# Kernel optimization log

Hardware: AMD Instinct MI355X
Metric: run time of the kernel (lower is better)

Reference implementation:

```python
import jax, jax.numpy as jnp
import numpy as np

B = 32; H = 56; W = 56; DIM = 192; WS = 7; SHIFT = 3; HEADS = 6
HEAD_DIM = DIM // HEADS; N = WS * WS; NW = (H // WS) * (W // WS)
HIDDEN = int(DIM * 4.0)
EPS = 1e-5


def _rel_pos_index():
    # standard Swin relative position index, shape (N, N), static
    coords = np.stack(np.meshgrid(np.arange(WS), np.arange(WS), indexing='ij'))  # (2, ws, ws)
    coords = coords.reshape(2, -1)                                               # (2, N)
    rel = (coords[:, :, None] - coords[:, None, :]).transpose(1, 2, 0)           # (N, N, 2)
    rel[:, :, 0] += WS - 1
    rel[:, :, 1] += WS - 1
    rel[:, :, 0] *= 2 * WS - 1
    return rel.sum(-1)  # (N, N)

REL_IDX = _rel_pos_index()


def _compute_attn_mask():
    # standard Swin SW-MSA mask, shape (NW, N, N), static
    img = np.zeros((H, W), dtype=np.float32)
    cnt = 0
    slices = (slice(0, -WS), slice(-WS, -SHIFT), slice(-SHIFT, None))
    for hs in slices:
        for ws_ in slices:
            img[hs, ws_] = cnt
            cnt += 1
    mw = img.reshape(H // WS, WS, W // WS, WS).transpose(0, 2, 1, 3).reshape(-1, N)  # (NW, N)
    diff = mw[:, None, :] - mw[:, :, None]
    return np.where(diff != 0, np.float32(-100.0), np.float32(0.0))


def _layernorm(x, g, b):
    mu = jnp.mean(x, axis=-1, keepdims=True)
    var = jnp.mean(jnp.square(x - mu), axis=-1, keepdims=True)
    return (x - mu) * jax.lax.rsqrt(var + EPS) * g + b


def setup_inputs() -> dict:
    key = jax.random.key(0)
    ks = jax.random.split(key, 8)
    s = 0.02
    inp = {
        'x': jax.random.normal(ks[0], (B, H * W, DIM), dtype=jnp.float32),
        'g1': jnp.ones((DIM,), jnp.float32), 'b1': jnp.zeros((DIM,), jnp.float32),
        'qkv_w': jax.random.normal(ks[1], (DIM, 3 * DIM), jnp.float32) * s,
        'qkv_b': jnp.zeros((3 * DIM,), jnp.float32),
        'proj_w': jax.random.normal(ks[2], (DIM, DIM), jnp.float32) * s,
        'proj_b': jnp.zeros((DIM,), jnp.float32),
        'rel_table': jax.random.normal(ks[3], ((2 * WS - 1) ** 2, HEADS), jnp.float32) * s,
        'g2': jnp.ones((DIM,), jnp.float32), 'b2': jnp.zeros((DIM,), jnp.float32),
        'fc1_w': jax.random.normal(ks[4], (DIM, HIDDEN), jnp.float32) * s,
        'fc1_b': jnp.zeros((HIDDEN,), jnp.float32),
        'fc2_w': jax.random.normal(ks[5], (HIDDEN, DIM), jnp.float32) * s,
        'fc2_b': jnp.zeros((DIM,), jnp.float32),
        'attn_mask': jnp.asarray(_compute_attn_mask()),
    }
    return inp


def reference(x, g1, b1, qkv_w, qkv_b, proj_w, proj_b, rel_table, g2, b2,
              fc1_w, fc1_b, fc2_w, fc2_b, attn_mask):
    shortcut = x
    h = _layernorm(x, g1, b1).reshape(B, H, W, DIM)
    h = jnp.roll(h, (-SHIFT, -SHIFT), axis=(1, 2))
    # window partition -> (B*NW, N, C)
    win = h.reshape(B, H // WS, WS, W // WS, WS, DIM).transpose(0, 1, 3, 2, 4, 5)
    win = win.reshape(-1, N, DIM)
    qkv = (win @ qkv_w + qkv_b).reshape(-1, N, 3, HEADS, HEAD_DIM).transpose(2, 0, 3, 1, 4)
    q, k, v = qkv[0], qkv[1], qkv[2]                         # (B*NW, heads, N, d)
    attn = jnp.einsum('whnd,whmd->whnm', q, k) * (HEAD_DIM ** -0.5)
    bias = rel_table[REL_IDX.reshape(-1)].reshape(N, N, HEADS).transpose(2, 0, 1)
    attn = attn + bias[None]
    attn = attn.reshape(B, NW, HEADS, N, N) + attn_mask[None, :, None]
    attn = jax.nn.softmax(attn, axis=-1).reshape(-1, HEADS, N, N)
    out = jnp.einsum('whnm,whmd->whnd', attn, v).transpose(0, 2, 1, 3).reshape(-1, N, DIM)
    out = out @ proj_w + proj_b
    # window reverse -> (B, H, W, C)
    out = out.reshape(B, H // WS, W // WS, WS, WS, DIM).transpose(0, 1, 3, 2, 4, 5)
    out = out.reshape(B, H, W, DIM)
    out = jnp.roll(out, (SHIFT, SHIFT), axis=(1, 2)).reshape(B, H * W, DIM)
    x = shortcut + out
    shortcut2 = x
    h = _layernorm(x, g2, b2)
    h = jax.nn.gelu(h @ fc1_w + fc1_b, approximate=False)
    h = h @ fc2_w + fc2_b
    return shortcut2 + h
```

## Files before the change

kernel.cpp:

```cpp
#include <hip/hip_runtime.h>
#include <math.h>

#define B_      32
#define HH      56
#define WW_     56
#define DIM     192
#define WS_     7
#define SHIFT_  3
#define HEADS   6
#define HDIM    32
#define NTOK    49
#define NWIN    64
#define HIDDEN  768
#define MTOT    (B_*HH*WW_)
#define CHUNK2  50176
#define EPS_    1e-5f
#define SCALE_  0.17677669529663687f

#define BK  32
#define LDK 40

#define ALD 200
#define PLD 36
#define VLD 68

typedef unsigned short u16;
typedef __attribute__((ext_vector_type(8))) __bf16 bf16x8;
typedef __attribute__((ext_vector_type(4))) float f32x4;

__device__ __forceinline__ float bf2f(u16 u) {
    union { unsigned int i; float f; } c; c.i = ((unsigned int)u) << 16; return c.f;
}
__device__ __forceinline__ u16 f2bf(float f) {
    union { float f; unsigned int i; } c; c.f = f;
    unsigned int x = c.i;
    return (u16)((x + 0x7FFFu + ((x >> 16) & 1u)) >> 16);
}

__device__ __forceinline__ float wave_sum(float v) {
    #pragma unroll
    for (int off = 32; off > 0; off >>= 1) v += __shfl_xor(v, off, 64);
    return v;
}

__global__ __launch_bounds__(256) void transpose_w_kernel(
        const float* __restrict__ W, u16* __restrict__ Wt, int K, int N) {
    __shared__ float t[32][33];
    int nt32 = N >> 5;
    int bx = blockIdx.x % nt32;
    int by = blockIdx.x / nt32;
    int tx = threadIdx.x & 31, ty = threadIdx.x >> 5;
    #pragma unroll
    for (int i = 0; i < 4; i++)
        t[ty + i * 8][tx] = W[(size_t)(by * 32 + ty + i * 8) * N + bx * 32 + tx];
    __syncthreads();
    #pragma unroll
    for (int i = 0; i < 4; i++)
        Wt[(size_t)(bx * 32 + ty + i * 8) * K + by * 32 + tx] = f2bf(t[tx][ty + i * 8]);
}

__global__ __launch_bounds__(256) void build_tbl_kernel(
        const float* __restrict__ rel_table, const float* __restrict__ mask,
        float* __restrict__ tbl) {
    int idx = blockIdx.x * 256 + threadIdx.x;
    int kj   = idx & 63;
    int qi   = (idx >> 6) & 63;
    int head = (idx >> 12) % 6;
    int wl   = idx / (6 << 12);
    float v;
    if (qi < NTOK && kj < NTOK) {
        int qr = qi / WS_, qc = qi % WS_;
        int kr = kj / WS_, kc = kj % WS_;
        int ri = (qr - kr + 6) * 13 + (qc - kc + 6);
        v = rel_table[ri * HEADS + head] + mask[((size_t)wl * NTOK + qi) * NTOK + kj];
    } else {
        v = -1e30f;
    }
    tbl[idx] = v;
}

__global__ __launch_bounds__(256) void ln1_window_kernel(
        const float* __restrict__ x, const float* __restrict__ g,
        const float* __restrict__ b, u16* __restrict__ out) {
    int row  = blockIdx.x * 4 + (threadIdx.x >> 6);
    int lane = threadIdx.x & 63;
    int win = row / NTOK;
    int n   = row - win * NTOK;
    int bb  = win >> 6;
    int wl  = win & 63;
    int hi  = (wl >> 3) * WS_ + n / WS_;
    int hj  = (wl & 7) * WS_ + n % WS_;
    int sh = hi + SHIFT_; if (sh >= HH) sh -= HH;
    int sw = hj + SHIFT_; if (sw >= WW_) sw -= WW_;
    const float* xr = x + ((size_t)(bb * HH * WW_ + sh * WW_ + sw)) * DIM;
    float v0 = xr[lane], v1 = xr[lane + 64], v2 = xr[lane + 128];
    float s  = wave_sum(v0 + v1 + v2);
    float sq = wave_sum(v0 * v0 + v1 * v1 + v2 * v2);
    float mu  = s * (1.0f / DIM);
    float var = sq * (1.0f / DIM) - mu * mu;
    float r = rsqrtf(var + EPS_);
    u16* orow = out + (size_t)row * DIM;
    orow[lane]       = f2bf((v0 - mu) * r * g[lane]       + b[lane]);
    orow[lane + 64]  = f2bf((v1 - mu) * r * g[lane + 64]  + b[lane + 64]);
    orow[lane + 128] = f2bf((v2 - mu) * r * g[lane + 128] + b[lane + 128]);
}

__global__ __launch_bounds__(256) void ln2_kernel(
        const float* __restrict__ x, const float* __restrict__ g,
        const float* __restrict__ b, u16* __restrict__ out) {
    int row  = blockIdx.x * 4 + (threadIdx.x >> 6);
    int lane = threadIdx.x & 63;
    const float* xr = x + (size_t)row * DIM;
    float v0 = xr[lane], v1 = xr[lane + 64], v2 = xr[lane + 128];
    float s  = wave_sum(v0 + v1 + v2);
    float sq = wave_sum(v0 * v0 + v1 * v1 + v2 * v2);
    float mu  = s * (1.0f / DIM);
    float var = sq * (1.0f / DIM) - mu * mu;
    float r = rsqrtf(var + EPS_);
    u16* orow = out + (size_t)row * DIM;
    orow[lane]       = f2bf((v0 - mu) * r * g[lane]       + b[lane]);
    orow[lane + 64]  = f2bf((v1 - mu) * r * g[lane + 64]  + b[lane + 64]);
    orow[lane + 128] = f2bf((v2 - mu) * r * g[lane + 128] + b[lane + 128]);
}

__global__ __launch_bounds__(384) void fused_attn_kernel(
        const u16* __restrict__ hwin, const u16* __restrict__ qkv_wT,
        const float* __restrict__ qkv_b, const u16* __restrict__ proj_wT,
        const float* __restrict__ proj_b, const float* __restrict__ tbl,
        const float* __restrict__ x, float* __restrict__ x1) {
    __shared__ u16 sm[26880];
    u16* R1 = sm;
    u16* Vt = sm + 13824;

    const int tid  = threadIdx.x;
    const int w    = tid >> 6;
    const int lane = tid & 63;
    const int lrow = lane & 15, lq = lane >> 4;
    const int win  = blockIdx.x;
    const int wl   = win & 63, bb = win >> 6;

    {
        const uint4* src = (const uint4*)(hwin + (size_t)win * NTOK * DIM);
        uint4 z; z.x = z.y = z.z = z.w = 0u;
        #pragma unroll
        for (int it = 0; it < 4; it++) {
            int i = tid + it * 384;
            int row = i / 24, c = i - row * 24;
            uint4 v = (row < NTOK) ? src[row * 24 + c] : z;
            *(uint4*)&R1[row * ALD + c * 8] = v;
        }
    }
    __syncthreads();

    f32x4 acc[3][4][2];
    #pragma unroll
    for (int o = 0; o < 3; o++)
        #pragma unroll
        for (int mt = 0; mt < 4; mt++)
            #pragma unroll
            for (int nt = 0; nt < 2; nt++) acc[o][mt][nt] = (f32x4){0.f, 0.f, 0.f, 0.f};

    const u16* bcol[3][2];
    #pragma unroll
    for (int o = 0; o < 3; o++)
        #pragma unroll
        for (int nt = 0; nt < 2; nt++)
            bcol[o][nt] = qkv_wT + (size_t)(o * DIM + w * 32 + nt * 16 + lrow) * DIM + lq * 8;

    #pragma unroll
    for (int ks = 0; ks < 6; ks++) {
        bf16x8 aF[4];
        #pragma unroll
        for (int mt = 0; mt < 4; mt++)
            aF[mt] = *(const bf16x8*)&R1[(mt * 16 + lrow) * ALD + ks * 32 + lq * 8];
        bf16x8 bF[3][2];
        #pragma unroll
        for (int o = 0; o < 3; o++)
            #pragma unroll
            for (int nt = 0; nt < 2; nt++)
                bF[o][nt] = *(const bf16x8*)(bcol[o][nt] + ks * 32);
        __builtin_amdgcn_s_setprio(1);
        #pragma unroll
        for (int o = 0; o < 3; o++)
            #pragma unroll
            for (int mt = 0; mt < 4; mt++)
                #pragma unroll
                for (int nt = 0; nt < 2; nt++)
                    acc[o][mt][nt] = __builtin_amdgcn_mfma_f32_16x16x32_bf16(
                        aF[mt], bF[o][nt], acc[o][mt][nt], 0, 0, 0);
        __builtin_amdgcn_s_setprio(0);
    }
    float bias_[3][2];
    #pragma unroll
    for (int o = 0; o < 3; o++)
        #pragma unroll
        for (int nt = 0; nt < 2; nt++)
            bias_[o][nt] = qkv_b[o * DIM + w * 32 + nt * 16 + lrow];
    #pragma unroll
    for (int o = 0; o < 3; o++)
        #pragma unroll
        for (int mt = 0; mt < 4; mt++)
            #pragma unroll
            for (int nt = 0; nt < 2; nt++)
                #pragma unroll
                for (int r = 0; r < 4; r++) acc[o][mt][nt][r] += bias_[o][nt];

    __syncthreads();

    #pragma unroll
    for (int mt = 0; mt < 4; mt++)
        #pragma unroll
        for (int nt = 0; nt < 2; nt++)
            #pragma unroll
            for (int r = 0; r < 4; r++)
                R1[(mt * 16 + lq * 4 + r) * ALD + w * 32 + nt * 16 + lrow] =
                    f2bf(acc[0][mt][nt][r]);
    bf16x8 qf[4];
    #pragma unroll
    for (int mt = 0; mt < 4; mt++)
        qf[mt] = *(const bf16x8*)&R1[(mt * 16 + lrow) * ALD + w * 32 + lq * 8];

    #pragma unroll
    for (int mt = 0; mt < 4; mt++)
        #pragma unroll
        for (int nt = 0; nt < 2; nt++)
            #pragma unroll
            for (int r = 0; r < 4; r++)
                R1[(mt * 16 + lq * 4 + r) * ALD + w * 32 + nt * 16 + lrow] =
                    f2bf(acc[1][mt][nt][r]);
    bf16x8 kf[4];
    #pragma unroll
    for (int nt = 0; nt < 4; nt++)
        kf[nt] = *(const bf16x8*)&R1[(nt * 16 + lrow) * ALD + w * 32 + lq * 8];

    #pragma unroll
    for (int mt = 0; mt < 4; mt++)
        #pragma unroll
        for (int nt = 0; nt < 2; nt++)
            #pragma unroll
            for (int r = 0; r < 4; r++)
                Vt[(w * 32 + nt * 16 + lrow) * VLD + mt * 16 + lq * 4 + r] =
                    f2bf(acc[2][mt][nt][r]);

    f32x4 sc[4][4];
    __builtin_amdgcn_s_setprio(1);
    #pragma unroll
    for (int mt = 0; mt < 4; mt++)
        #pragma unroll
        for (int nt = 0; nt < 4; nt++) {
            f32x4 z = (f32x4){0.f, 0.f, 0.f, 0.f};
            sc[mt][nt] = __builtin_amdgcn_mfma_f32_16x16x32_bf16(qf[mt], kf[nt], z, 0, 0, 0);
        }
    __builtin_amdgcn_s_setprio(0);
    const float* tb = tbl + (((size_t)wl * HEADS + w) << 12);
    float inv[4][4];
    #pragma unroll
    for (int mt = 0; mt < 4; mt++)
        #pragma unroll
        for (int r = 0; r < 4; r++) {
            int qi = mt * 16 + lq * 4 + r;
            float mx = -3.0e38f;
            #pragma unroll
            for (int nt = 0; nt < 4; nt++) {
                float s = sc[mt][nt][r] * SCALE_ + tb[(qi << 6) + nt * 16 + lrow];
                sc[mt][nt][r] = s;
                mx = fmaxf(mx, s);
            }
            #pragma unroll
            for (int off = 8; off > 0; off >>= 1) mx = fmaxf(mx, __shfl_xor(mx, off, 64));
            float sum = 0.f;
            #pragma unroll
            for (int nt = 0; nt < 4; nt++) {
                float e = __expf(sc[mt][nt][r] - mx);
                sc[mt][nt][r] = e;
                sum += e;
            }
            #pragma unroll
            for (int off = 8; off > 0; off >>= 1) sum += __shfl_xor(sum, off, 64);
            inv[mt][r] = 1.0f / sum;
        }

    u16* Pl = R1 + w * (64 * PLD);
    f32x4 oc[4][2];
    #pragma unroll
    for (int mt = 0; mt < 4; mt++)
        #pragma unroll
        for (int nd = 0; nd < 2; nd++) oc[mt][nd] = (f32x4){0.f, 0.f, 0.f, 0.f};
    #pragma unroll
    for (int ks = 0; ks < 2; ks++) {
        #pragma unroll
        for (int mt = 0; mt < 4; mt++)
            #pragma unroll
            for (int ntl = 0; ntl < 2; ntl++)
                #pragma unroll
                for (int r = 0; r < 4; r++)
                    Pl[(mt * 16 + lq * 4 + r) * PLD + ntl * 16 + lrow] =
                        f2bf(sc[mt][ks * 2 + ntl][r]);
        bf16x8 vf[2];
        #pragma unroll
        for (int nd = 0; nd < 2; nd++)
            vf[nd] = *(const bf16x8*)&Vt[(w * 32 + nd * 16 + lrow) * VLD + ks * 32 + lq * 8];
        __builtin_amdgcn_s_setprio(1);
        #pragma unroll
        for (int mt = 0; mt < 4; mt++) {
            bf16x8 pf = *(const bf16x8*)&Pl[(mt * 16 + lrow) * PLD + lq * 8];
            #pragma unroll
            for (int nd = 0; nd < 2; nd++)
                oc[mt][nd] = __builtin_amdgcn_mfma_f32_16x16x32_bf16(pf, vf[nd],
                                                                     oc[mt][nd], 0, 0, 0);
        }
        __builtin_amdgcn_s_setprio(0);
    }
    __syncthreads();

    #pragma unroll
    for (int mt = 0; mt < 4; mt++)
        #pragma unroll
        for (int nd = 0; nd < 2; nd++)
            #pragma unroll
            for (int r = 0; r < 4; r++)
                R1[(mt * 16 + lq * 4 + r) * ALD + w * 32 + nd * 16 + lrow] =
                    f2bf(oc[mt][nd][r] * inv[mt][r]);
    __syncthreads();

    f32x4 pacc[4][2];
    #pragma unroll
    for (int mt = 0; mt < 4; mt++)
        #pragma unroll
        for (int nt = 0; nt < 2; nt++) pacc[mt][nt] = (f32x4){0.f, 0.f, 0.f, 0.f};
    const u16* pcol[2];
    #pragma unroll
    for (int nt = 0; nt < 2; nt++)
        pcol[nt] = proj_wT + (size_t)(w * 32 + nt * 16 + lrow) * DIM + lq * 8;
    #pragma unroll
    for (int ks = 0; ks < 6; ks++) {
        bf16x8 af[4];
        #pragma unroll
        for (int mt = 0; mt < 4; mt++)
            af[mt] = *(const bf16x8*)&R1[(mt * 16 + lrow) * ALD + ks * 32 + lq * 8];
        bf16x8 pb[2];
        #pragma unroll
        for (int nt = 0; nt < 2; nt++) pb[nt] = *(const bf16x8*)(pcol[nt] + ks * 32);
        __builtin_amdgcn_s_setprio(1);
        #pragma unroll
        for (int mt = 0; mt < 4; mt++)
            #pragma unroll
            for (int nt = 0; nt < 2; nt++)
                pacc[mt][nt] = __builtin_amdgcn_mfma_f32_16x16x32_bf16(
                    af[mt], pb[nt], pacc[mt][nt], 0, 0, 0);
        __builtin_amdgcn_s_setprio(0);
    }
    float pbias[2];
    #pragma unroll
    for (int nt = 0; nt < 2; nt++) pbias[nt] = proj_b[w * 32 + nt * 16 + lrow];
    #pragma unroll
    for (int mt = 0; mt < 4; mt++)
        #pragma unroll
        for (int r = 0; r < 4; r++) {
            int n = mt * 16 + lq * 4 + r;
            if (n < NTOK) {
                int hi = (wl >> 3) * WS_ + n / WS_;
                int hj = (wl & 7) * WS_ + n % WS_;
                int dh = hi + SHIFT_; if (dh >= HH) dh -= HH;
                int dw = hj + SHIFT_; if (dw >= WW_) dw -= WW_;
                size_t tok = (size_t)(bb * HH * WW_ + dh * WW_ + dw);
                #pragma unroll
                for (int nt = 0; nt < 2; nt++) {
                    int col = w * 32 + nt * 16 + lrow;
                    x1[tok * DIM + col] = x[tok * DIM + col] + pacc[mt][nt][r] + pbias[nt];
                }
            }
        }
}

template<int K, int BM_, int BN_, int WR, int MT>
__device__ __forceinline__ void gemm_core2(
        const u16* __restrict__ A, const u16* __restrict__ Bt,
        int m0, int n0, u16 (*As)[BM_][LDK], u16 (*Bs)[BN_][LDK],
        f32x4 (&acc)[MT][4]) {
    constexpr int WC = 4 / WR;
    constexpr int AL = BM_ / 64;
    constexpr int BL = BN_ / 64;
    const int tid  = threadIdx.x;
    const int lane = tid & 63, w = tid >> 6;
    const int lrow = lane & 15, lq = lane >> 4;
    const int wrow = (w / WC) * (MT * 16);
    const int wcol = (w % WC) * 64;
    const int am = tid >> 2, ako = (tid & 3) * 8;

    #pragma unroll
    for (int i = 0; i < MT; i++)
        #pragma unroll
        for (int j = 0; j < 4; j++) acc[i][j] = (f32x4){0.f, 0.f, 0.f, 0.f};

    uint4 a_ld[AL], b_ld[BL];
    auto load_tile = [&](int k0) {
        #pragma unroll
        for (int i = 0; i < AL; i++)
            a_ld[i] = *(const uint4*)(A + (size_t)(m0 + am + i * 64) * K + k0 + ako);
        #pragma unroll
        for (int i = 0; i < BL; i++)
            b_ld[i] = *(const uint4*)(Bt + (size_t)(n0 + am + i * 64) * K + k0 + ako);
    };
    auto store_tile = [&](int buf) {
        #pragma unroll
        for (int i = 0; i < AL; i++) *(uint4*)&As[buf][am + i * 64][ako] = a_ld[i];
        #pragma unroll
        for (int i = 0; i < BL; i++) *(uint4*)&Bs[buf][am + i * 64][ako] = b_ld[i];
    };

    load_tile(0);
    store_tile(0);
    __syncthreads();
    int cur = 0;
    for (int k0 = 0; k0 < K; k0 += BK) {
        const bool more = (k0 + BK) < K;
        if (more) load_tile(k0 + BK);
        bf16x8 aF[MT], bF[4];
        #pragma unroll
        for (int mt = 0; mt < MT; mt++)
            aF[mt] = *(const bf16x8*)&As[cur][wrow + mt * 16 + lrow][lq * 8];
        #pragma unroll
        for (int nt = 0; nt < 4; nt++)
            bF[nt] = *(const bf16x8*)&Bs[cur][wcol + nt * 16 + lrow][lq * 8];
        #pragma unroll
        for (int mt = 0; mt < MT; mt++)
            #pragma unroll
            for (int nt = 0; nt < 4; nt++)
                acc[mt][nt] = __builtin_amdgcn_mfma_f32_16x16x32_bf16(
                    aF[mt], bF[nt], acc[mt][nt], 0, 0, 0);
        if (more) store_tile(cur ^ 1);
        __syncthreads();
        cur ^= 1;
    }
}

__global__ __launch_bounds__(256) void gemm_fc1_mfma(
        const u16* __restrict__ Aact, const u16* __restrict__ Bt,
        const float* __restrict__ bias, u16* __restrict__ fc1_out) {
    __shared__ u16 As[2][128][LDK];
    __shared__ u16 Bs[2][128][LDK];
    f32x4 acc[4][4];
    int m0 = blockIdx.y * 128, n0 = blockIdx.x * 128;
    gemm_core2<DIM, 128, 128, 2, 4>(Aact, Bt, m0, n0, As, Bs, acc);
    int lane = threadIdx.x & 63, w = threadIdx.x >> 6;
    int lrow = lane & 15, lq = lane >> 4;
    int wrow = (w >> 1) * 64, wcol = (w & 1) * 64;
    #pragma unroll
    for (int nt = 0; nt < 4; nt++) {
        int col = n0 + wcol + nt * 16 + lrow;
        float bv = bias[col];
        #pragma unroll
        for (int mt = 0; mt < 4; mt++)
            #pragma unroll
            for (int r = 0; r < 4; r++) {
                size_t row = (size_t)(m0 + wrow + mt * 16 + lq * 4 + r);
                float val = acc[mt][nt][r] + bv;
                float gel = 0.5f * val * (1.0f + erff(val * 0.70710678118f));
                fc1_out[row * HIDDEN + col] = f2bf(gel);
            }
    }
}

__global__ __launch_bounds__(256) void gemm_fc2_mfma(
        const u16* __restrict__ Aact, const u16* __restrict__ Bt,
        const float* __restrict__ bias, float* __restrict__ out, int row_off) {
    __shared__ u16 As[2][128][LDK];
    __shared__ u16 Bs[2][64][LDK];
    f32x4 acc[2][4];
    int m0 = blockIdx.y * 128, n0 = blockIdx.x * 64;
    gemm_core2<HIDDEN, 128, 64, 4, 2>(Aact, Bt, m0, n0, As, Bs, acc);
    int lane = threadIdx.x & 63, w = threadIdx.x >> 6;
    int lrow = lane & 15, lq = lane >> 4;
    int wrow = w * 32;
    #pragma unroll
    for (int nt = 0; nt < 4; nt++) {
        int col = n0 + nt * 16 + lrow;
        float bv = bias[col];
        #pragma unroll
        for (int mt = 0; mt < 2; mt++)
            #pragma unroll
            for (int r = 0; r < 4; r++) {
                size_t grow = (size_t)(row_off + m0 + wrow + mt * 16 + lq * 4 + r);
                out[grow * DIM + col] = out[grow * DIM + col] + acc[mt][nt][r] + bv;
            }
    }
}

extern "C" void kernel_launch(void* const* d_in, const int* in_sizes, int n_in,
                              void* d_out, int out_size, void* d_ws, size_t ws_size,
                              hipStream_t stream) {
    const float* x         = (const float*)d_in[0];
    const float* g1        = (const float*)d_in[1];
    const float* b1        = (const float*)d_in[2];
    const float* qkv_w     = (const float*)d_in[3];
    const float* qkv_b     = (const float*)d_in[4];
    const float* proj_w    = (const float*)d_in[5];
    const float* proj_b    = (const float*)d_in[6];
    const float* rel_table = (const float*)d_in[7];
    const float* g2        = (const float*)d_in[8];
    const float* b2        = (const float*)d_in[9];
    const float* fc1_w     = (const float*)d_in[10];
    const float* fc1_b     = (const float*)d_in[11];
    const float* fc2_w     = (const float*)d_in[12];
    const float* fc2_b     = (const float*)d_in[13];
    const float* attn_mask = (const float*)d_in[14];
    float* out = (float*)d_out;

    const size_t S = (size_t)MTOT * DIM;
    u16* wsu = (u16*)d_ws;
    u16*   hwin    = wsu;
    u16*   fc1_buf = wsu + S;
    u16*   wT      = wsu + 3 * S;
    u16*   qkv_wT  = wT;
    u16*   proj_wT = wT + 110592;
    u16*   fc1_wT  = wT + 147456;
    u16*   fc2_wT  = wT + 294912;
    float* tbl     = (float*)(wT + 442368);

    transpose_w_kernel<<<(DIM / 32) * (3 * DIM / 32), 256, 0, stream>>>(qkv_w, qkv_wT, DIM, 3 * DIM);
    transpose_w_kernel<<<(DIM / 32) * (DIM / 32), 256, 0, stream>>>(proj_w, proj_wT, DIM, DIM);
    transpose_w_kernel<<<(DIM / 32) * (HIDDEN / 32), 256, 0, stream>>>(fc1_w, fc1_wT, DIM, HIDDEN);
    transpose_w_kernel<<<(HIDDEN / 32) * (DIM / 32), 256, 0, stream>>>(fc2_w, fc2_wT, HIDDEN, DIM);
    build_tbl_kernel<<<(NWIN * HEADS * 64 * 64) / 256, 256, 0, stream>>>(rel_table, attn_mask, tbl);

    ln1_window_kernel<<<MTOT / 4, 256, 0, stream>>>(x, g1, b1, hwin);
    fused_attn_kernel<<<B_ * NWIN, 384, 0, stream>>>(hwin, qkv_wT, qkv_b, proj_wT, proj_b,
                                                     tbl, x, out);
    ln2_kernel<<<MTOT / 4, 256, 0, stream>>>(out, g2, b2, hwin);
    for (int c = 0; c < 2; c++) {
        const u16* h2c = hwin + (size_t)c * CHUNK2 * DIM;
        gemm_fc1_mfma<<<dim3(HIDDEN / 128, CHUNK2 / 128), 256, 0, stream>>>(h2c, fc1_wT, fc1_b, fc1_buf);
        gemm_fc2_mfma<<<dim3(DIM / 64, CHUNK2 / 128), 256, 0, stream>>>(fc1_buf, fc2_wT, fc2_b,
                                                                        out, c * CHUNK2);
    }
}
```

Before: 583.3 us.

## Fuse MLP fc1+GELU+fc2 into one kernel keeping hidden activations in LDS

Replaces the chunked fc1 and fc2 GEMM launches with a single kernel per 32-row tile. The tile computes fc1 with GELU into shared memory and then fc2 from that buffer, so the large bf16 hidden activation never goes through global memory. Weight fragments are read directly from global or L2 with no LDS staging, and setprio is wrapped around the MFMA bursts. The attention kernel's LDS padding (PLD/VLD) is also changed. The tradeoff is a small M tile with heavy per-block weight re-reads from cache, which lowers arithmetic intensity.

```diff
diff --git a/kernel.cpp b/kernel.cpp
--- a/kernel.cpp
+++ b/kernel.cpp
@@ -13,16 +13,15 @@
 #define NWIN    64
 #define HIDDEN  768
 #define MTOT    (B_*HH*WW_)
-#define CHUNK2  50176
 #define EPS_    1e-5f
 #define SCALE_  0.17677669529663687f
 
-#define BK  32
-#define LDK 40
-
 #define ALD 200
-#define PLD 36
-#define VLD 68
+#define PLD 40
+#define VLD 72
+
+#define MROWS 32
+#define HLD   776
 
 typedef unsigned short u16;
 typedef __attribute__((ext_vector_type(8))) __bf16 bf16x8;
@@ -128,9 +127,9 @@
         const float* __restrict__ qkv_b, const u16* __restrict__ proj_wT,
         const float* __restrict__ proj_b, const float* __restrict__ tbl,
         const float* __restrict__ x, float* __restrict__ x1) {
-    __shared__ u16 sm[26880];
+    __shared__ u16 sm[29184];
     u16* R1 = sm;
-    u16* Vt = sm + 13824;
+    u16* Vt = sm + 15360;
 
     const int tid  = threadIdx.x;
     const int w    = tid >> 6;
@@ -373,116 +372,110 @@
         }
 }
 
-template<int K, int BM_, int BN_, int WR, int MT>
-__device__ __forceinline__ void gemm_core2(
-        const u16* __restrict__ A, const u16* __restrict__ Bt,
-        int m0, int n0, u16 (*As)[BM_][LDK], u16 (*Bs)[BN_][LDK],
-        f32x4 (&acc)[MT][4]) {
-    constexpr int WC = 4 / WR;
-    constexpr int AL = BM_ / 64;
-    constexpr int BL = BN_ / 64;
+__global__ __launch_bounds__(384) void mlp_fused_kernel(
+        const u16* __restrict__ h2, const u16* __restrict__ fc1_wT,
+        const float* __restrict__ fc1_b, const u16* __restrict__ fc2_wT,
+        const float* __restrict__ fc2_b, float* __restrict__ out) {
+    __shared__ u16 Ash[MROWS * ALD];
+    __shared__ u16 Hsh[MROWS * HLD];
+
     const int tid  = threadIdx.x;
-    const int lane = tid & 63, w = tid >> 6;
+    const int w    = tid >> 6;
+    const int lane = tid & 63;
     const int lrow = lane & 15, lq = lane >> 4;
-    const int wrow = (w / WC) * (MT * 16);
-    const int wcol = (w % WC) * 64;
-    const int am = tid >> 2, ako = (tid & 3) * 8;
-
-    #pragma unroll
-    for (int i = 0; i < MT; i++)
-        #pragma unroll
-        for (int j = 0; j < 4; j++) acc[i][j] = (f32x4){0.f, 0.f, 0.f, 0.f};
-
-    uint4 a_ld[AL], b_ld[BL];
-    auto load_tile = [&](int k0) {
-        #pragma unroll
-        for (int i = 0; i < AL; i++)
-            a_ld[i] = *(const uint4*)(A + (size_t)(m0 + am + i * 64) * K + k0 + ako);
-        #pragma unroll
-        for (int i = 0; i < BL; i++)
-            b_ld[i] = *(const uint4*)(Bt + (size_t)(n0 + am + i * 64) * K + k0 + ako);
-    };
-    auto store_tile = [&](int buf) {
-        #pragma unroll
-        for (int i = 0; i < AL; i++) *(uint4*)&As[buf][am + i * 64][ako] = a_ld[i];
-        #pragma unroll
-        for (int i = 0; i < BL; i++) *(uint4*)&Bs[buf][am + i * 64][ako] = b_ld[i];
-    };
-
-    load_tile(0);
-    store_tile(0);
-    __syncthreads();
-    int cur = 0;
-    for (int k0 = 0; k0 < K; k0 += BK) {
-        const bool more = (k0 + BK) < K;
-        if (more) load_tile(k0 + BK);
-        bf16x8 aF[MT], bF[4];
-        #pragma unroll
-        for (int mt = 0; mt < MT; mt++)
-            aF[mt] = *(const bf16x8*)&As[cur][wrow + mt * 16 + lrow][lq * 8];
-        #pragma unroll
-        for (int nt = 0; nt < 4; nt++)
-            bF[nt] = *(const bf16x8*)&Bs[cur][wcol + nt * 16 + lrow][lq * 8];
-        #pragma unroll
-        for (int mt = 0; mt < MT; mt++)
-            #pragma unroll
-            for (int nt = 0; nt < 4; nt++)
-                acc[mt][nt] = __builtin_amdgcn_mfma_f32_16x16x32_bf16(
-                    aF[mt], bF[nt], acc[mt][nt], 0, 0, 0);
-        if (more) store_tile(cur ^ 1);
-        __syncthreads();
-        cur ^= 1;
-    }
-}
-
-__global__ __launch_bounds__(256) void gemm_fc1_mfma(
-        const u16* __restrict__ Aact, const u16* __restrict__ Bt,
-        const float* __restrict__ bias, u16* __restrict__ fc1_out) {
-    __shared__ u16 As[2][128][LDK];
-    __shared__ u16 Bs[2][128][LDK];
-    f32x4 acc[4][4];
-    int m0 = blockIdx.y * 128, n0 = blockIdx.x * 128;
-    gemm_core2<DIM, 128, 128, 2, 4>(Aact, Bt, m0, n0, As, Bs, acc);
-    int lane = threadIdx.x & 63, w = threadIdx.x >> 6;
-    int lrow = lane & 15, lq = lane >> 4;
-    int wrow = (w >> 1) * 64, wcol = (w & 1) * 64;
-    #pragma unroll
-    for (int nt = 0; nt < 4; nt++) {
-        int col = n0 + wcol + nt * 16 + lrow;
-        float bv = bias[col];
-        #pragma unroll
-        for (int mt = 0; mt < 4; mt++)
+    const int m0   = blockIdx.x * MROWS;
+
+    {
+        const uint4* src = (const uint4*)(h2 + (size_t)m0 * DIM);
+        #pragma unroll
+        for (int it = 0; it < 2; it++) {
+            int i = tid + it * 384;
+            int row = i / 24, c = i - row * 24;
+            *(uint4*)&Ash[row * ALD + c * 8] = src[row * 24 + c];
+        }
+    }
+    __syncthreads();
+
+    f32x4 hacc[2][8];
+    #pragma unroll
+    for (int mt = 0; mt < 2; mt++)
+        #pragma unroll
+        for (int nt = 0; nt < 8; nt++) hacc[mt][nt] = (f32x4){0.f, 0.f, 0.f, 0.f};
+    const u16* b1col[8];
+    #pragma unroll
+    for (int nt = 0; nt < 8; nt++)
+        b1col[nt] = fc1_wT + (size_t)(w * 128 + nt * 16 + lrow) * DIM + lq * 8;
+
+    #pragma unroll
+    for (int ks = 0; ks < 6; ks++) {
+        bf16x8 aF[2];
+        #pragma unroll
+        for (int mt = 0; mt < 2; mt++)
+            aF[mt] = *(const bf16x8*)&Ash[(mt * 16 + lrow) * ALD + ks * 32 + lq * 8];
+        bf16x8 bF[8];
+        #pragma unroll
+        for (int nt = 0; nt < 8; nt++) bF[nt] = *(const bf16x8*)(b1col[nt] + ks * 32);
+        __builtin_amdgcn_s_setprio(1);
+        #pragma unroll
+        for (int mt = 0; mt < 2; mt++)
+            #pragma unroll
+            for (int nt = 0; nt < 8; nt++)
+                hacc[mt][nt] = __builtin_amdgcn_mfma_f32_16x16x32_bf16(
+                    aF[mt], bF[nt], hacc[mt][nt], 0, 0, 0);
+        __builtin_amdgcn_s_setprio(0);
+    }
+    #pragma unroll
+    for (int nt = 0; nt < 8; nt++) {
+        float bv = fc1_b[w * 128 + nt * 16 + lrow];
+        #pragma unroll
+        for (int mt = 0; mt < 2; mt++)
             #pragma unroll
             for (int r = 0; r < 4; r++) {
-                size_t row = (size_t)(m0 + wrow + mt * 16 + lq * 4 + r);
-                float val = acc[mt][nt][r] + bv;
+                float val = hacc[mt][nt][r] + bv;
                 float gel = 0.5f * val * (1.0f + erff(val * 0.70710678118f));
-                fc1_out[row * HIDDEN + col] = f2bf(gel);
+                Hsh[(mt * 16 + lq * 4 + r) * HLD + w * 128 + nt * 16 + lrow] = f2bf(gel);
             }
     }
-}
-
-__global__ __launch_bounds__(256) void gemm_fc2_mfma(
-        const u16* __restrict__ Aact, const u16* __restrict__ Bt,
-        const float* __restrict__ bias, float* __restrict__ out, int row_off) {
-    __shared__ u16 As[2][128][LDK];
-    __shared__ u16 Bs[2][64][LDK];
-    f32x4 acc[2][4];
-    int m0 = blockIdx.y * 128, n0 = blockIdx.x * 64;
-    gemm_core2<HIDDEN, 128, 64, 4, 2>(Aact, Bt, m0, n0, As, Bs, acc);
-    int lane = threadIdx.x & 63, w = threadIdx.x >> 6;
-    int lrow = lane & 15, lq = lane >> 4;
-    int wrow = w * 32;
-    #pragma unroll
-    for (int nt = 0; nt < 4; nt++) {
-        int col = n0 + nt * 16 + lrow;
-        float bv = bias[col];
+    __syncthreads();
+
+    f32x4 acc2[2][2];
+    #pragma unroll
+    for (int mt = 0; mt < 2; mt++)
+        #pragma unroll
+        for (int nt = 0; nt < 2; nt++) acc2[mt][nt] = (f32x4){0.f, 0.f, 0.f, 0.f};
+    const u16* b2col[2];
+    #pragma unroll
+    for (int nt = 0; nt < 2; nt++)
+        b2col[nt] = fc2_wT + (size_t)(w * 32 + nt * 16 + lrow) * HIDDEN + lq * 8;
+
+    #pragma unroll 4
+    for (int ks = 0; ks < 24; ks++) {
+        bf16x8 hF[2];
         #pragma unroll
         for (int mt = 0; mt < 2; mt++)
+            hF[mt] = *(const bf16x8*)&Hsh[(mt * 16 + lrow) * HLD + ks * 32 + lq * 8];
+        bf16x8 b2F[2];
+        #pragma unroll
+        for (int nt = 0; nt < 2; nt++) b2F[nt] = *(const bf16x8*)(b2col[nt] + ks * 32);
+        __builtin_amdgcn_s_setprio(1);
+        #pragma unroll
+        for (int mt = 0; mt < 2; mt++)
+            #pragma unroll
+            for (int nt = 0; nt < 2; nt++)
+                acc2[mt][nt] = __builtin_amdgcn_mfma_f32_16x16x32_bf16(
+                    hF[mt], b2F[nt], acc2[mt][nt], 0, 0, 0);
+        __builtin_amdgcn_s_setprio(0);
+    }
+    #pragma unroll
+    for (int nt = 0; nt < 2; nt++) {
+        int col = w * 32 + nt * 16 + lrow;
+        float bv = fc2_b[col];
+        #pragma unroll
+        for (int mt = 0; mt < 2; mt++)
             #pragma unroll
             for (int r = 0; r < 4; r++) {
-                size_t grow = (size_t)(row_off + m0 + wrow + mt * 16 + lq * 4 + r);
-                out[grow * DIM + col] = out[grow * DIM + col] + acc[mt][nt][r] + bv;
+                size_t grow = (size_t)(m0 + mt * 16 + lq * 4 + r);
+                out[grow * DIM + col] = out[grow * DIM + col] + acc2[mt][nt][r] + bv;
             }
     }
 }
@@ -510,8 +503,7 @@
     const size_t S = (size_t)MTOT * DIM;
     u16* wsu = (u16*)d_ws;
     u16*   hwin    = wsu;
-    u16*   fc1_buf = wsu + S;
-    u16*   wT      = wsu + 3 * S;
+    u16*   wT      = wsu + S;
     u16*   qkv_wT  = wT;
     u16*   proj_wT = wT + 110592;
     u16*   fc1_wT  = wT + 147456;
@@ -528,10 +520,5 @@
     fused_attn_kernel<<<B_ * NWIN, 384, 0, stream>>>(hwin, qkv_wT, qkv_b, proj_wT, proj_b,
                                                      tbl, x, out);
     ln2_kernel<<<MTOT / 4, 256, 0, stream>>>(out, g2, b2, hwin);
-    for (int c = 0; c < 2; c++) {
-        const u16* h2c = hwin + (size_t)c * CHUNK2 * DIM;
-        gemm_fc1_mfma<<<dim3(HIDDEN / 128, CHUNK2 / 128), 256, 0, stream>>>(h2c, fc1_wT, fc1_b, fc1_buf);
-        gemm_fc2_mfma<<<dim3(DIM / 64, CHUNK2 / 128), 256, 0, stream>>>(fc1_buf, fc2_wT, fc2_b,
-                                                                        out, c * CHUNK2);
-    }
-}
+    mlp_fused_kernel<<<MTOT / MROWS, 384, 0, stream>>>(hwin, fc1_wT, fc1_b, fc2_wT, fc2_b, out);
+}
```

Measured after the change: 625.9 us. 7.3% more time.
